# Kernel optimization log

Measured on AMD Instinct MI355X. Metric: run time of the kernel, lower is better.

Reference implementation:

```python
import jax, jax.numpy as jnp
import numpy as np

B, N, C_IN, C_OUT, R_IN, R_OUT, NUM_PSI, E = 4, 1024, 128, 256, 32, 32, 2, 65536


def psi(x, src, dst, W, b):
    # GIN-style GNN layer: aggregate neighbors via scatter-add, then linear+relu
    agg = jax.ops.segment_sum(x[src], dst, num_segments=x.shape[0])
    return jax.nn.relu((x + agg) @ W + b)


def setup_inputs() -> dict:
    key = jax.random.key(0)
    ks = jax.random.split(key, 12)
    inp = {
        'x_s': jax.random.normal(ks[0], (B * N, C_IN), jnp.float32),
        'edge_index_s': jax.random.randint(ks[1], (2, E), 0, B * N, jnp.int32),
        'x_t': jax.random.normal(ks[2], (B * N, C_IN), jnp.float32),
        'edge_index_t': jax.random.randint(ks[3], (2, E), 0, B * N, jnp.int32),
        'r': jax.random.normal(ks[4], (NUM_PSI, B, N, R_IN), jnp.float32),
        'W1': jax.random.normal(ks[5], (C_IN, C_OUT), jnp.float32) * (0.2 / np.sqrt(C_IN)),
        'b1': jnp.zeros((C_OUT,), jnp.float32),
        'Wp': jax.random.normal(ks[6], (NUM_PSI, R_IN, R_OUT), jnp.float32) * (1.0 / np.sqrt(R_IN)),
        'bp': jnp.zeros((NUM_PSI, R_OUT), jnp.float32),
        'Wm1': jax.random.normal(ks[7], (R_OUT, R_OUT), jnp.float32) * (1.0 / np.sqrt(R_OUT)),
        'bm1': jnp.zeros((R_OUT,), jnp.float32),
        'Wm2': jax.random.normal(ks[8], (R_OUT, 1), jnp.float32) * (1.0 / np.sqrt(R_OUT)),
        'bm2': jnp.zeros((1,), jnp.float32),
        'sum_weights': jnp.ones((NUM_PSI + 1,), jnp.float32),
    }
    return inp


def reference(x_s, edge_index_s, x_t, edge_index_t, r, W1, b1, Wp, bp, Wm1, bm1, Wm2, bm2, sum_weights):
    src_s, dst_s = edge_index_s[0], edge_index_s[1]
    src_t, dst_t = edge_index_t[0], edge_index_t[1]
    # psi_1 node embeddings, then dense-batch (equal-size graphs -> masks all true)
    h_s = psi(x_s, src_s, dst_s, W1, b1).reshape(B, N, C_OUT)
    h_t = psi(x_t, src_t, dst_t, W1, b1).reshape(B, N, C_OUT)
    S_hat = jnp.einsum('bsc,btc->bst', h_s, h_t)  # [B, N_s, N_t]
    S_0 = jax.nn.softmax(S_hat, axis=-1)
    S_stack = []
    for i in range(NUM_PSI):  # structurally distinct psi modules
        S = jax.nn.softmax(S_hat, axis=-1)
        r_s = r[i]  # [B, N, R_IN] random node indicators
        r_t = jnp.einsum('bst,bsr->btr', S, r_s)
        o_s = psi(r_s.reshape(B * N, R_IN), src_s, dst_s, Wp[i], bp[i]).reshape(B, N, R_OUT)
        o_t = psi(r_t.reshape(B * N, R_IN), src_t, dst_t, Wp[i], bp[i]).reshape(B, N, R_OUT)
        D = o_s[:, :, None, :] - o_t[:, None, :, :]  # [B, N_s, N_t, R_OUT]
        upd = (jax.nn.relu(D @ Wm1 + bm1) @ Wm2 + bm2)[..., 0]
        S_hat = S_hat + upd
        S_stack.append(jax.nn.softmax(S_hat, axis=-1))
    S_final = sum_weights[0] * S_0
    for i in range(NUM_PSI):
        S_final = S_final + sum_weights[i + 1] * S_stack[i]
    return jax.nn.softmax(S_final.reshape(B * N, N), axis=-1)
```

## Files before the change

### kernel.cpp

```cpp
#include <hip/hip_runtime.h>
#include <hip/hip_bf16.h>

#define NBATCH 4
#define NSEQ   1024
#define BNN    4096
#define CIN    128
#define COUT   256
#define RDIM   32
#define NEDGE  65536

__global__ void edge_hist(const int* __restrict__ ei_s, const int* __restrict__ ei_t,
                          int* __restrict__ cnt) {
    int gid = blockIdx.x * blockDim.x + threadIdx.x;
    int list = gid >> 16;
    int e = gid & (NEDGE - 1);
    const int* ei = list ? ei_t : ei_s;
    atomicAdd(&cnt[list * BNN + ei[NEDGE + e]], 1);
}

__global__ void edge_scan(const int* __restrict__ cnt, int* __restrict__ offs,
                          int* __restrict__ cursor) {
    __shared__ int sums[256];
    int list = blockIdx.x;
    int tid = threadIdx.x;
    int local[16];
    int s = 0;
#pragma unroll
    for (int k = 0; k < 16; k++) { local[k] = cnt[list * BNN + tid * 16 + k]; s += local[k]; }
    sums[tid] = s;
    __syncthreads();
    for (int off = 1; off < 256; off <<= 1) {
        int v = 0;
        if (tid >= off) v = sums[tid - off];
        __syncthreads();
        if (tid >= off) sums[tid] += v;
        __syncthreads();
    }
    int run = tid ? sums[tid - 1] : 0;
#pragma unroll
    for (int k = 0; k < 16; k++) {
        offs[list * (BNN + 1) + tid * 16 + k] = run;
        cursor[list * BNN + tid * 16 + k] = run;
        run += local[k];
    }
    if (tid == 255) offs[list * (BNN + 1) + BNN] = run;
}

__global__ void edge_place(const int* __restrict__ ei_s, const int* __restrict__ ei_t,
                           int* __restrict__ cursor, int* __restrict__ ssrc) {
    int gid = blockIdx.x * blockDim.x + threadIdx.x;
    int list = gid >> 16;
    int e = gid & (NEDGE - 1);
    const int* ei = list ? ei_t : ei_s;
    int dst = ei[NEDGE + e], src = ei[e];
    int p = atomicAdd(&cursor[list * BNN + dst], 1);
    ssrc[list * NEDGE + p] = src;
}

__global__ void gather_agg128(const float* __restrict__ x_s, const float* __restrict__ x_t,
                              const int* __restrict__ offs, const int* __restrict__ ssrc,
                              float* __restrict__ t_s, float* __restrict__ t_t) {
    __shared__ int sl[128];
    int node = blockIdx.x & (BNN - 1);
    int list = blockIdx.x >> 12;
    const float* x = list ? x_t : x_s;
    float* t = list ? t_t : t_s;
    int c = threadIdx.x;
    int beg = offs[list * (BNN + 1) + node], end = offs[list * (BNN + 1) + node + 1];
    float acc = x[(size_t)node * CIN + c];
    for (int base = beg; base < end; base += 128) {
        int cnt = min(128, end - base);
        __syncthreads();
        if (c < cnt) sl[c] = ssrc[list * NEDGE + base + c];
        __syncthreads();
        int e = 0;
        for (; e + 4 <= cnt; e += 4) {
            int n0 = sl[e], n1 = sl[e + 1], n2 = sl[e + 2], n3 = sl[e + 3];
            acc += x[(size_t)n0 * CIN + c] + x[(size_t)n1 * CIN + c]
                 + x[(size_t)n2 * CIN + c] + x[(size_t)n3 * CIN + c];
        }
        for (; e < cnt; e++) acc += x[(size_t)sl[e] * CIN + c];
    }
    t[(size_t)node * CIN + c] = acc;
}

__global__ void gather_agg32(const float* __restrict__ rs, const float* __restrict__ rtin,
                             const int* __restrict__ offs, const int* __restrict__ ssrc,
                             float* __restrict__ trs, float* __restrict__ trt) {
    int list = blockIdx.y;
    int node = blockIdx.x * 8 + (threadIdx.x >> 5);
    int c = threadIdx.x & 31;
    const float* in = list ? rtin : rs;
    float* outp = list ? trt : trs;
    int beg = offs[list * (BNN + 1) + node], end = offs[list * (BNN + 1) + node + 1];
    float acc = in[(size_t)node * RDIM + c];
    for (int e = beg; e < end; e++)
        acc += in[(size_t)ssrc[list * NEDGE + e] * RDIM + c];
    outp[(size_t)node * RDIM + c] = acc;
}

__global__ void psi1_gemm(const float* __restrict__ t_s, const float* __restrict__ t_t,
                          const float* __restrict__ W1, const float* __restrict__ b1,
                          float* __restrict__ h_s, float* __restrict__ h_t) {
    __shared__ float rows[8][CIN];
    int half = blockIdx.x >> 9;
    const float* t = half ? t_t : t_s;
    float* h = half ? h_t : h_s;
    int r0 = (blockIdx.x & 511) * 8;
    int tid = threadIdx.x;
    {
        int rr = tid >> 5, c4 = (tid & 31) << 2;
        *(float4*)&rows[rr][c4] = *(const float4*)(t + (size_t)(r0 + rr) * CIN + c4);
    }
    __syncthreads();
    float acc[8];
    float bias = b1[tid];
#pragma unroll
    for (int r = 0; r < 8; r++) acc[r] = bias;
    for (int k = 0; k < CIN; k++) {
        float w = W1[k * COUT + tid];
#pragma unroll
        for (int r = 0; r < 8; r++) acc[r] = fmaf(rows[r][k], w, acc[r]);
    }
#pragma unroll
    for (int r = 0; r < 8; r++)
        h[(size_t)(r0 + r) * COUT + tid] = fmaxf(acc[r], 0.f);
}

__global__ __launch_bounds__(256) void shat_gemm(const float* __restrict__ hs,
                                                 const float* __restrict__ ht,
                                                 float* __restrict__ Sh) {
    __shared__ float As[16][132];
    __shared__ float Bs[16][132];
    int b  = blockIdx.z;
    int s0 = blockIdx.y * 128, t0 = blockIdx.x * 128;
    const float* A  = hs + (size_t)b * NSEQ * COUT;
    const float* Bm = ht + (size_t)b * NSEQ * COUT;
    int tid = threadIdx.x;
    int tx = tid & 15, ty = tid >> 4;
    int lr = tid >> 1;
    int lk = (tid & 1) * 8;
    const float* Ap = A  + (size_t)(s0 + lr) * COUT + lk;
    const float* Bp = Bm + (size_t)(t0 + lr) * COUT + lk;
    float4 a0 = *(const float4*)(Ap);
    float4 a1 = *(const float4*)(Ap + 4);
    float4 b0 = *(const float4*)(Bp);
    float4 b1 = *(const float4*)(Bp + 4);
    float acc[8][8] = {};
    for (int kp = 0; kp < 16; kp++) {
        __syncthreads();
        As[lk + 0][lr] = a0.x; As[lk + 1][lr] = a0.y; As[lk + 2][lr] = a0.z; As[lk + 3][lr] = a0.w;
        As[lk + 4][lr] = a1.x; As[lk + 5][lr] = a1.y; As[lk + 6][lr] = a1.z; As[lk + 7][lr] = a1.w;
        Bs[lk + 0][lr] = b0.x; Bs[lk + 1][lr] = b0.y; Bs[lk + 2][lr] = b0.z; Bs[lk + 3][lr] = b0.w;
        Bs[lk + 4][lr] = b1.x; Bs[lk + 5][lr] = b1.y; Bs[lk + 6][lr] = b1.z; Bs[lk + 7][lr] = b1.w;
        __syncthreads();
        if (kp < 15) {
            a0 = *(const float4*)(Ap + (kp + 1) * 16);
            a1 = *(const float4*)(Ap + (kp + 1) * 16 + 4);
            b0 = *(const float4*)(Bp + (kp + 1) * 16);
            b1 = *(const float4*)(Bp + (kp + 1) * 16 + 4);
        }
#pragma unroll
        for (int k = 0; k < 16; k++) {
            float av[8], bv[8];
            *(float4*)&av[0] = *(const float4*)&As[k][ty * 8];
            *(float4*)&av[4] = *(const float4*)&As[k][ty * 8 + 4];
            *(float4*)&bv[0] = *(const float4*)&Bs[k][tx * 8];
            *(float4*)&bv[4] = *(const float4*)&Bs[k][tx * 8 + 4];
#pragma unroll
            for (int i = 0; i < 8; i++)
#pragma unroll
                for (int j = 0; j < 8; j++)
                    acc[i][j] = fmaf(av[i], bv[j], acc[i][j]);
        }
    }
#pragma unroll
    for (int i = 0; i < 8; i++) {
#pragma unroll
        for (int j4 = 0; j4 < 8; j4 += 4) {
            float4 v = make_float4(acc[i][j4], acc[i][j4 + 1], acc[i][j4 + 2], acc[i][j4 + 3]);
            *(float4*)(Sh + ((size_t)b * NSEQ + s0 + ty * 8 + i) * NSEQ + t0 + tx * 8 + j4) = v;
        }
    }
}

__global__ void softmax_acc2(const float* __restrict__ Sh, float* __restrict__ Sfin,
                             const float* __restrict__ sw, float* __restrict__ mstat,
                             float* __restrict__ istat, int widx, int init) {
    int row = blockIdx.x, tid = threadIdx.x;
    float4 v = *(const float4*)(Sh + (size_t)row * NSEQ + tid * 4);
    float m = fmaxf(fmaxf(v.x, v.y), fmaxf(v.z, v.w));
#pragma unroll
    for (int o = 32; o; o >>= 1) m = fmaxf(m, __shfl_xor(m, o));
    __shared__ float redm[4], reds[4];
    int wid = tid >> 6, lane = tid & 63;
    if (lane == 0) redm[wid] = m;
    __syncthreads();
    m = fmaxf(fmaxf(redm[0], redm[1]), fmaxf(redm[2], redm[3]));
    float4 e;
    e.x = __expf(v.x - m); e.y = __expf(v.y - m);
    e.z = __expf(v.z - m); e.w = __expf(v.w - m);
    float s = e.x + e.y + e.z + e.w;
#pragma unroll
    for (int o = 32; o; o >>= 1) s += __shfl_xor(s, o);
    if (lane == 0) reds[wid] = s;
    __syncthreads();
    s = reds[0] + reds[1] + reds[2] + reds[3];
    float inv = 1.0f / s;
    float w = sw[widx] * inv;
    float* fp = Sfin + (size_t)row * NSEQ + tid * 4;
    float4 f;
    if (init) {
        f = make_float4(w * e.x, w * e.y, w * e.z, w * e.w);
    } else {
        float4 old = *(const float4*)fp;
        f = make_float4(fmaf(w, e.x, old.x), fmaf(w, e.y, old.y),
                        fmaf(w, e.z, old.z), fmaf(w, e.w, old.w));
    }
    *(float4*)fp = f;
    if (tid == 0) { mstat[row] = m; istat[row] = inv; }
}

__global__ void softmax_final(const float* __restrict__ Sh, const float* __restrict__ Sfin,
                              const float* __restrict__ sw, float* __restrict__ out) {
    int row = blockIdx.x, tid = threadIdx.x;
    __shared__ float redm[4], reds[4], redm2[4], reds2[4];
    int wid = tid >> 6, lane = tid & 63;
    float4 v = *(const float4*)(Sh + (size_t)row * NSEQ + tid * 4);
    float m = fmaxf(fmaxf(v.x, v.y), fmaxf(v.z, v.w));
#pragma unroll
    for (int o = 32; o; o >>= 1) m = fmaxf(m, __shfl_xor(m, o));
    if (lane == 0) redm[wid] = m;
    __syncthreads();
    m = fmaxf(fmaxf(redm[0], redm[1]), fmaxf(redm[2], redm[3]));
    float4 e;
    e.x = __expf(v.x - m); e.y = __expf(v.y - m);
    e.z = __expf(v.z - m); e.w = __expf(v.w - m);
    float s = e.x + e.y + e.z + e.w;
#pragma unroll
    for (int o = 32; o; o >>= 1) s += __shfl_xor(s, o);
    if (lane == 0) reds[wid] = s;
    __syncthreads();
    s = reds[0] + reds[1] + reds[2] + reds[3];
    float w = sw[2] / s;
    float4 old = *(const float4*)(Sfin + (size_t)row * NSEQ + tid * 4);
    float4 f = make_float4(fmaf(w, e.x, old.x), fmaf(w, e.y, old.y),
                           fmaf(w, e.z, old.z), fmaf(w, e.w, old.w));
    float m2 = fmaxf(fmaxf(f.x, f.y), fmaxf(f.z, f.w));
#pragma unroll
    for (int o = 32; o; o >>= 1) m2 = fmaxf(m2, __shfl_xor(m2, o));
    if (lane == 0) redm2[wid] = m2;
    __syncthreads();
    m2 = fmaxf(fmaxf(redm2[0], redm2[1]), fmaxf(redm2[2], redm2[3]));
    float4 e2;
    e2.x = __expf(f.x - m2); e2.y = __expf(f.y - m2);
    e2.z = __expf(f.z - m2); e2.w = __expf(f.w - m2);
    float s2 = e2.x + e2.y + e2.z + e2.w;
#pragma unroll
    for (int o = 32; o; o >>= 1) s2 += __shfl_xor(s2, o);
    if (lane == 0) reds2[wid] = s2;
    __syncthreads();
    s2 = reds2[0] + reds2[1] + reds2[2] + reds2[3];
    float inv2 = 1.0f / s2;
    float4 sv = make_float4(e2.x * inv2, e2.y * inv2, e2.z * inv2, e2.w * inv2);
    *(float4*)(out + (size_t)row * NSEQ + tid * 4) = sv;
}

__global__ void rt_part(const float* __restrict__ Sh, const float* __restrict__ mstat,
                        const float* __restrict__ istat, const float* __restrict__ rs,
                        float* __restrict__ part) {
    __shared__ float rsld[64][33];
    __shared__ float ml[64], il[64];
    int b = blockIdx.z, t0 = blockIdx.y * 128, s0 = blockIdx.x * 64;
    int tid = threadIdx.x;
    if (tid < 64) ml[tid] = mstat[b * NSEQ + s0 + tid];
    else if (tid < 128) il[tid - 64] = istat[b * NSEQ + s0 + tid - 64];
#pragma unroll
    for (int q = 0; q < 2; q++) {
        int lid = (tid << 1) + q;
        int srow = lid >> 3, c4 = (lid & 7) << 2;
        float4 v = *(const float4*)(rs + ((size_t)b * NSEQ + s0 + srow) * RDIM + c4);
        rsld[srow][c4] = v.x; rsld[srow][c4 + 1] = v.y;
        rsld[srow][c4 + 2] = v.z; rsld[srow][c4 + 3] = v.w;
    }
    __syncthreads();
    int t = t0 + (tid & 127);
    int j0 = (tid >> 7) << 4;
    float acc[16] = {};
    const float* Sp = Sh + ((size_t)b * NSEQ + s0) * NSEQ + t;
#pragma unroll 8
    for (int s = 0; s < 64; s++) {
        float p = __expf(Sp[(size_t)s * NSEQ] - ml[s]) * il[s];
#pragma unroll
        for (int j = 0; j < 16; j++) acc[j] = fmaf(p, rsld[s][j0 + j], acc[j]);
    }
    float* pp = part + (((size_t)blockIdx.x * NBATCH + b) * NSEQ + t) * RDIM + j0;
#pragma unroll
    for (int j4 = 0; j4 < 16; j4 += 4)
        *(float4*)(pp + j4) = make_float4(acc[j4], acc[j4 + 1], acc[j4 + 2], acc[j4 + 3]);
}

__global__ void rt_reduce(const float* __restrict__ part, float* __restrict__ rt) {
    int i = blockIdx.x * blockDim.x + threadIdx.x;
    const float4* p = (const float4*)part + i;
    float4 a = make_float4(0.f, 0.f, 0.f, 0.f);
#pragma unroll
    for (int c = 0; c < 16; c++) {
        float4 v = p[(size_t)c * (BNN * RDIM / 4)];
        a.x += v.x; a.y += v.y; a.z += v.z; a.w += v.w;
    }
    ((float4*)rt)[i] = a;
}

__global__ void psi_r(const float* __restrict__ trs, const float* __restrict__ trt,
                      const float* __restrict__ Wp, const float* __restrict__ bp,
                      const float* __restrict__ Wm1, const float* __restrict__ bm1,
                      float* __restrict__ Ps, float* __restrict__ Pt) {
    __shared__ float sWp[32 * 32], sWm1[32 * 32];
    __shared__ float srow[8][33], so[8][33];
    int which = blockIdx.y;
    const float* t_r = which ? trt : trs;
    float* P = which ? Pt : Ps;
    int tid = threadIdx.x;
#pragma unroll
    for (int q = 0; q < 4; q++) {
        sWp[tid + q * 256]  = Wp[tid + q * 256];
        sWm1[tid + q * 256] = Wm1[tid + q * 256];
    }
    int g = tid >> 5, j = tid & 31;
    int row = blockIdx.x * 8 + g;
    srow[g][j] = t_r[(size_t)row * RDIM + j];
    __syncthreads();
    float acc = bp[j];
#pragma unroll
    for (int k = 0; k < 32; k++) acc = fmaf(srow[g][k], sWp[k * 32 + j], acc);
    float o = fmaxf(acc, 0.f);
    so[g][j] = o;
    __syncthreads();
    float acc2 = which ? 0.f : bm1[j];
#pragma unroll
    for (int k = 0; k < 32; k++) acc2 = fmaf(so[g][k], sWm1[k * 32 + j], acc2);
    P[(size_t)row * RDIM + j] = acc2;
}

__global__ void upd_add(const float* __restrict__ Ps, const float* __restrict__ Pt,
                        const float* __restrict__ Wm2, const float* __restrict__ bm2p,
                        float* __restrict__ Sh) {
    __shared__ float sPs[64][33], sPt[64][33];
    __shared__ float swm[32];
    int b = blockIdx.z, s0 = blockIdx.y * 64, t0 = blockIdx.x * 64;
    int tid = threadIdx.x;
#pragma unroll
    for (int q = 0; q < 2; q++) {
        int lid = (tid << 1) + q, rr = lid >> 3, c4 = (lid & 7) << 2;
        float4 a = *(const float4*)(Ps + ((size_t)b * NSEQ + s0 + rr) * RDIM + c4);
        sPs[rr][c4] = a.x; sPs[rr][c4 + 1] = a.y; sPs[rr][c4 + 2] = a.z; sPs[rr][c4 + 3] = a.w;
        float4 c = *(const float4*)(Pt + ((size_t)b * NSEQ + t0 + rr) * RDIM + c4);
        sPt[rr][c4] = c.x; sPt[rr][c4 + 1] = c.y; sPt[rr][c4 + 2] = c.z; sPt[rr][c4 + 3] = c.w;
    }
    if (tid < 32) swm[tid] = Wm2[tid];
    __syncthreads();
    float bm2 = bm2p[0];
    int tx = tid & 15, ty = tid >> 4;
    float acc[4][4] = {};
#pragma unroll
    for (int k = 0; k < 32; k++) {
        float w = swm[k];
        float ps[4], pt[4];
#pragma unroll
        for (int i = 0; i < 4; i++) ps[i] = sPs[ty * 4 + i][k];
#pragma unroll
        for (int j = 0; j < 4; j++) pt[j] = sPt[tx * 4 + j][k];
#pragma unroll
        for (int i = 0; i < 4; i++)
#pragma unroll
            for (int j = 0; j < 4; j++)
                acc[i][j] = fmaf(fmaxf(ps[i] - pt[j], 0.f), w, acc[i][j]);
    }
#pragma unroll
    for (int i = 0; i < 4; i++) {
        size_t base = ((size_t)b * NSEQ + s0 + ty * 4 + i) * NSEQ + t0 + tx * 4;
        float4 old = *(const float4*)(Sh + base);
        old.x += acc[i][0] + bm2; old.y += acc[i][1] + bm2;
        old.z += acc[i][2] + bm2; old.w += acc[i][3] + bm2;
        *(float4*)(Sh + base) = old;
    }
}

extern "C" void kernel_launch(void* const* d_in, const int* in_sizes, int n_in,
                              void* d_out, int out_size, void* d_ws, size_t ws_size,
                              hipStream_t stream) {
    const float* x_s  = (const float*)d_in[0];
    const int*   ei_s = (const int*)  d_in[1];
    const float* x_t  = (const float*)d_in[2];
    const int*   ei_t = (const int*)  d_in[3];
    const float* r    = (const float*)d_in[4];
    const float* W1   = (const float*)d_in[5];
    const float* b1   = (const float*)d_in[6];
    const float* Wp   = (const float*)d_in[7];
    const float* bp   = (const float*)d_in[8];
    const float* Wm1  = (const float*)d_in[9];
    const float* bm1  = (const float*)d_in[10];
    const float* Wm2  = (const float*)d_in[11];
    const float* bm2  = (const float*)d_in[12];
    const float* sw   = (const float*)d_in[13];
    float* out = (float*)d_out;

    float* ws = (float*)d_ws;
    float* t_s  = ws;  ws += (size_t)BNN * CIN;
    float* t_t  = ws;  ws += (size_t)BNN * CIN;
    float* h_s  = ws;  ws += (size_t)BNN * COUT;
    float* h_t  = ws;  ws += (size_t)BNN * COUT;
    float* Sh   = ws;  ws += (size_t)NBATCH * NSEQ * NSEQ;
    float* Sfin = ws;  ws += (size_t)NBATCH * NSEQ * NSEQ;
    float* mstat = ws; ws += BNN;
    float* istat = ws; ws += BNN;
    float* rt   = ws;  ws += (size_t)BNN * RDIM;
    float* trs  = ws;  ws += (size_t)BNN * RDIM;
    float* trt  = ws;  ws += (size_t)BNN * RDIM;
    float* Ps   = ws;  ws += (size_t)BNN * RDIM;
    float* Pt   = ws;  ws += (size_t)BNN * RDIM;
    int* icnt  = (int*)ws;
    int* ioffs = icnt  + 2 * BNN;
    int* icur  = ioffs + 2 * (BNN + 1);
    int* issrc = icur  + 2 * BNN;
    float* rtpart = h_s;

    hipMemsetAsync(icnt, 0, 2 * BNN * sizeof(int), stream);
    edge_hist <<<512, 256, 0, stream>>>(ei_s, ei_t, icnt);
    edge_scan <<<2, 256, 0, stream>>>(icnt, ioffs, icur);
    edge_place<<<512, 256, 0, stream>>>(ei_s, ei_t, icur, issrc);

    gather_agg128<<<8192, 128, 0, stream>>>(x_s, x_t, ioffs, issrc, t_s, t_t);
    psi1_gemm<<<1024, 256, 0, stream>>>(t_s, t_t, W1, b1, h_s, h_t);
    shat_gemm<<<dim3(8, 8, 4), 256, 0, stream>>>(h_s, h_t, Sh);

    for (int i = 0; i < 2; i++) {
        softmax_acc2<<<4096, 256, 0, stream>>>(Sh, Sfin, sw, mstat, istat, i, i == 0 ? 1 : 0);
        rt_part<<<dim3(16, 8, 4), 256, 0, stream>>>(Sh, mstat, istat,
                                                    r + (size_t)i * BNN * RDIM, rtpart);
        rt_reduce<<<128, 256, 0, stream>>>(rtpart, rt);
        gather_agg32<<<dim3(512, 2), 256, 0, stream>>>(r + (size_t)i * BNN * RDIM, rt,
                                                       ioffs, issrc, trs, trt);
        psi_r<<<dim3(512, 2), 256, 0, stream>>>(trs, trt, Wp + i * RDIM * RDIM,
                                                bp + i * RDIM, Wm1, bm1, Ps, Pt);
        upd_add<<<dim3(16, 16, 4), 256, 0, stream>>>(Ps, Pt, Wm2, bm2, Sh);
    }
    softmax_final<<<4096, 256, 0, stream>>>(Sh, Sfin, sw, out);
}
```

Before: 223.5 us.

## Keep per-stage S_hat buffers and fuse all weighted softmaxes into final pass

Instead of accumulating the weighted softmax sum into a separate Sfin buffer at every stage, each stage's S_hat is written to its own buffer and only per-row max and inverse-sum statistics are stored. A single final kernel recomputes the three softmaxes from the saved buffers, combines them and applies the outer softmax. This drops the Sfin read-modify-write passes at the cost of reading three full matrices at the end and using more workspace. The S_hat GEMM tile is also narrowed to 128x64, doubling the block count for better occupancy with less register reuse per thread.

```diff
diff --git a/kernel.cpp b/kernel.cpp
--- a/kernel.cpp
+++ b/kernel.cpp
@@ -131,62 +131,57 @@
                                                  const float* __restrict__ ht,
                                                  float* __restrict__ Sh) {
     __shared__ float As[16][132];
-    __shared__ float Bs[16][132];
+    __shared__ float Bs[16][68];
     int b  = blockIdx.z;
-    int s0 = blockIdx.y * 128, t0 = blockIdx.x * 128;
+    int s0 = blockIdx.y * 128, t0 = blockIdx.x * 64;
     const float* A  = hs + (size_t)b * NSEQ * COUT;
     const float* Bm = ht + (size_t)b * NSEQ * COUT;
     int tid = threadIdx.x;
     int tx = tid & 15, ty = tid >> 4;
-    int lr = tid >> 1;
-    int lk = (tid & 1) * 8;
-    const float* Ap = A  + (size_t)(s0 + lr) * COUT + lk;
-    const float* Bp = Bm + (size_t)(t0 + lr) * COUT + lk;
+    int lrA = tid >> 1,  lkA = (tid & 1) * 8;
+    int lrB = tid >> 2,  lkB = (tid & 3) * 4;
+    const float* Ap = A  + (size_t)(s0 + lrA) * COUT + lkA;
+    const float* Bp = Bm + (size_t)(t0 + lrB) * COUT + lkB;
     float4 a0 = *(const float4*)(Ap);
     float4 a1 = *(const float4*)(Ap + 4);
     float4 b0 = *(const float4*)(Bp);
-    float4 b1 = *(const float4*)(Bp + 4);
-    float acc[8][8] = {};
+    float acc[8][4] = {};
     for (int kp = 0; kp < 16; kp++) {
         __syncthreads();
-        As[lk + 0][lr] = a0.x; As[lk + 1][lr] = a0.y; As[lk + 2][lr] = a0.z; As[lk + 3][lr] = a0.w;
-        As[lk + 4][lr] = a1.x; As[lk + 5][lr] = a1.y; As[lk + 6][lr] = a1.z; As[lk + 7][lr] = a1.w;
-        Bs[lk + 0][lr] = b0.x; Bs[lk + 1][lr] = b0.y; Bs[lk + 2][lr] = b0.z; Bs[lk + 3][lr] = b0.w;
-        Bs[lk + 4][lr] = b1.x; Bs[lk + 5][lr] = b1.y; Bs[lk + 6][lr] = b1.z; Bs[lk + 7][lr] = b1.w;
+        As[lkA + 0][lrA] = a0.x; As[lkA + 1][lrA] = a0.y;
+        As[lkA + 2][lrA] = a0.z; As[lkA + 3][lrA] = a0.w;
+        As[lkA + 4][lrA] = a1.x; As[lkA + 5][lrA] = a1.y;
+        As[lkA + 6][lrA] = a1.z; As[lkA + 7][lrA] = a1.w;
+        Bs[lkB + 0][lrB] = b0.x; Bs[lkB + 1][lrB] = b0.y;
+        Bs[lkB + 2][lrB] = b0.z; Bs[lkB + 3][lrB] = b0.w;
         __syncthreads();
         if (kp < 15) {
             a0 = *(const float4*)(Ap + (kp + 1) * 16);
             a1 = *(const float4*)(Ap + (kp + 1) * 16 + 4);
             b0 = *(const float4*)(Bp + (kp + 1) * 16);
-            b1 = *(const float4*)(Bp + (kp + 1) * 16 + 4);
         }
 #pragma unroll
         for (int k = 0; k < 16; k++) {
-            float av[8], bv[8];
+            float av[8], bv[4];
             *(float4*)&av[0] = *(const float4*)&As[k][ty * 8];
             *(float4*)&av[4] = *(const float4*)&As[k][ty * 8 + 4];
-            *(float4*)&bv[0] = *(const float4*)&Bs[k][tx * 8];
-            *(float4*)&bv[4] = *(const float4*)&Bs[k][tx * 8 + 4];
+            *(float4*)&bv[0] = *(const float4*)&Bs[k][tx * 4];
 #pragma unroll
             for (int i = 0; i < 8; i++)
 #pragma unroll
-                for (int j = 0; j < 8; j++)
+                for (int j = 0; j < 4; j++)
                     acc[i][j] = fmaf(av[i], bv[j], acc[i][j]);
         }
     }
 #pragma unroll
     for (int i = 0; i < 8; i++) {
-#pragma unroll
-        for (int j4 = 0; j4 < 8; j4 += 4) {
-            float4 v = make_float4(acc[i][j4], acc[i][j4 + 1], acc[i][j4 + 2], acc[i][j4 + 3]);
-            *(float4*)(Sh + ((size_t)b * NSEQ + s0 + ty * 8 + i) * NSEQ + t0 + tx * 8 + j4) = v;
-        }
-    }
-}
-
-__global__ void softmax_acc2(const float* __restrict__ Sh, float* __restrict__ Sfin,
-                             const float* __restrict__ sw, float* __restrict__ mstat,
-                             float* __restrict__ istat, int widx, int init) {
+        float4 v = make_float4(acc[i][0], acc[i][1], acc[i][2], acc[i][3]);
+        *(float4*)(Sh + ((size_t)b * NSEQ + s0 + ty * 8 + i) * NSEQ + t0 + tx * 4) = v;
+    }
+}
+
+__global__ void softmax_stats(const float* __restrict__ Sh, float* __restrict__ mstat,
+                              float* __restrict__ istat) {
     int row = blockIdx.x, tid = threadIdx.x;
     float4 v = *(const float4*)(Sh + (size_t)row * NSEQ + tid * 4);
     float m = fmaxf(fmaxf(v.x, v.y), fmaxf(v.z, v.w));
@@ -197,72 +192,71 @@
     if (lane == 0) redm[wid] = m;
     __syncthreads();
     m = fmaxf(fmaxf(redm[0], redm[1]), fmaxf(redm[2], redm[3]));
-    float4 e;
-    e.x = __expf(v.x - m); e.y = __expf(v.y - m);
-    e.z = __expf(v.z - m); e.w = __expf(v.w - m);
-    float s = e.x + e.y + e.z + e.w;
+    float s = __expf(v.x - m) + __expf(v.y - m) + __expf(v.z - m) + __expf(v.w - m);
 #pragma unroll
     for (int o = 32; o; o >>= 1) s += __shfl_xor(s, o);
     if (lane == 0) reds[wid] = s;
     __syncthreads();
-    s = reds[0] + reds[1] + reds[2] + reds[3];
-    float inv = 1.0f / s;
-    float w = sw[widx] * inv;
-    float* fp = Sfin + (size_t)row * NSEQ + tid * 4;
+    if (tid == 0) {
+        float tot = reds[0] + reds[1] + reds[2] + reds[3];
+        mstat[row] = m;
+        istat[row] = 1.0f / tot;
+    }
+}
+
+__global__ void softmax_final3(const float* __restrict__ Sh0, const float* __restrict__ Sh1,
+                               const float* __restrict__ Sh2, const float* __restrict__ m0a,
+                               const float* __restrict__ i0a, const float* __restrict__ m1a,
+                               const float* __restrict__ i1a, const float* __restrict__ sw,
+                               float* __restrict__ out) {
+    int row = blockIdx.x, tid = threadIdx.x;
+    __shared__ float red[4];
+    int wid = tid >> 6, lane = tid & 63;
+    float4 v0 = *(const float4*)(Sh0 + (size_t)row * NSEQ + tid * 4);
+    float4 v1 = *(const float4*)(Sh1 + (size_t)row * NSEQ + tid * 4);
+    float4 v2 = *(const float4*)(Sh2 + (size_t)row * NSEQ + tid * 4);
+    float m2 = fmaxf(fmaxf(v2.x, v2.y), fmaxf(v2.z, v2.w));
+#pragma unroll
+    for (int o = 32; o; o >>= 1) m2 = fmaxf(m2, __shfl_xor(m2, o));
+    if (lane == 0) red[wid] = m2;
+    __syncthreads();
+    m2 = fmaxf(fmaxf(red[0], red[1]), fmaxf(red[2], red[3]));
+    __syncthreads();
+    float4 e2;
+    e2.x = __expf(v2.x - m2); e2.y = __expf(v2.y - m2);
+    e2.z = __expf(v2.z - m2); e2.w = __expf(v2.w - m2);
+    float s2 = e2.x + e2.y + e2.z + e2.w;
+#pragma unroll
+    for (int o = 32; o; o >>= 1) s2 += __shfl_xor(s2, o);
+    if (lane == 0) red[wid] = s2;
+    __syncthreads();
+    s2 = red[0] + red[1] + red[2] + red[3];
+    __syncthreads();
+    float w0 = sw[0] * i0a[row], w1 = sw[1] * i1a[row], w2 = sw[2] / s2;
+    float m0 = m0a[row], m1 = m1a[row];
     float4 f;
-    if (init) {
-        f = make_float4(w * e.x, w * e.y, w * e.z, w * e.w);
-    } else {
-        float4 old = *(const float4*)fp;
-        f = make_float4(fmaf(w, e.x, old.x), fmaf(w, e.y, old.y),
-                        fmaf(w, e.z, old.z), fmaf(w, e.w, old.w));
-    }
-    *(float4*)fp = f;
-    if (tid == 0) { mstat[row] = m; istat[row] = inv; }
-}
-
-__global__ void softmax_final(const float* __restrict__ Sh, const float* __restrict__ Sfin,
-                              const float* __restrict__ sw, float* __restrict__ out) {
-    int row = blockIdx.x, tid = threadIdx.x;
-    __shared__ float redm[4], reds[4], redm2[4], reds2[4];
-    int wid = tid >> 6, lane = tid & 63;
-    float4 v = *(const float4*)(Sh + (size_t)row * NSEQ + tid * 4);
-    float m = fmaxf(fmaxf(v.x, v.y), fmaxf(v.z, v.w));
-#pragma unroll
-    for (int o = 32; o; o >>= 1) m = fmaxf(m, __shfl_xor(m, o));
-    if (lane == 0) redm[wid] = m;
-    __syncthreads();
-    m = fmaxf(fmaxf(redm[0], redm[1]), fmaxf(redm[2], redm[3]));
-    float4 e;
-    e.x = __expf(v.x - m); e.y = __expf(v.y - m);
-    e.z = __expf(v.z - m); e.w = __expf(v.w - m);
-    float s = e.x + e.y + e.z + e.w;
-#pragma unroll
-    for (int o = 32; o; o >>= 1) s += __shfl_xor(s, o);
-    if (lane == 0) reds[wid] = s;
-    __syncthreads();
-    s = reds[0] + reds[1] + reds[2] + reds[3];
-    float w = sw[2] / s;
-    float4 old = *(const float4*)(Sfin + (size_t)row * NSEQ + tid * 4);
-    float4 f = make_float4(fmaf(w, e.x, old.x), fmaf(w, e.y, old.y),
-                           fmaf(w, e.z, old.z), fmaf(w, e.w, old.w));
-    float m2 = fmaxf(fmaxf(f.x, f.y), fmaxf(f.z, f.w));
-#pragma unroll
-    for (int o = 32; o; o >>= 1) m2 = fmaxf(m2, __shfl_xor(m2, o));
-    if (lane == 0) redm2[wid] = m2;
-    __syncthreads();
-    m2 = fmaxf(fmaxf(redm2[0], redm2[1]), fmaxf(redm2[2], redm2[3]));
-    float4 e2;
-    e2.x = __expf(f.x - m2); e2.y = __expf(f.y - m2);
-    e2.z = __expf(f.z - m2); e2.w = __expf(f.w - m2);
-    float s2 = e2.x + e2.y + e2.z + e2.w;
-#pragma unroll
-    for (int o = 32; o; o >>= 1) s2 += __shfl_xor(s2, o);
-    if (lane == 0) reds2[wid] = s2;
-    __syncthreads();
-    s2 = reds2[0] + reds2[1] + reds2[2] + reds2[3];
-    float inv2 = 1.0f / s2;
-    float4 sv = make_float4(e2.x * inv2, e2.y * inv2, e2.z * inv2, e2.w * inv2);
+    f.x = fmaf(w0, __expf(v0.x - m0), fmaf(w1, __expf(v1.x - m1), w2 * e2.x));
+    f.y = fmaf(w0, __expf(v0.y - m0), fmaf(w1, __expf(v1.y - m1), w2 * e2.y));
+    f.z = fmaf(w0, __expf(v0.z - m0), fmaf(w1, __expf(v1.z - m1), w2 * e2.z));
+    f.w = fmaf(w0, __expf(v0.w - m0), fmaf(w1, __expf(v1.w - m1), w2 * e2.w));
+    float mf = fmaxf(fmaxf(f.x, f.y), fmaxf(f.z, f.w));
+#pragma unroll
+    for (int o = 32; o; o >>= 1) mf = fmaxf(mf, __shfl_xor(mf, o));
+    if (lane == 0) red[wid] = mf;
+    __syncthreads();
+    mf = fmaxf(fmaxf(red[0], red[1]), fmaxf(red[2], red[3]));
+    __syncthreads();
+    float4 ef;
+    ef.x = __expf(f.x - mf); ef.y = __expf(f.y - mf);
+    ef.z = __expf(f.z - mf); ef.w = __expf(f.w - mf);
+    float sf = ef.x + ef.y + ef.z + ef.w;
+#pragma unroll
+    for (int o = 32; o; o >>= 1) sf += __shfl_xor(sf, o);
+    if (lane == 0) red[wid] = sf;
+    __syncthreads();
+    sf = red[0] + red[1] + red[2] + red[3];
+    float inv = 1.0f / sf;
+    float4 sv = make_float4(ef.x * inv, ef.y * inv, ef.z * inv, ef.w * inv);
     *(float4*)(out + (size_t)row * NSEQ + tid * 4) = sv;
 }
 
@@ -345,7 +339,7 @@
 
 __global__ void upd_add(const float* __restrict__ Ps, const float* __restrict__ Pt,
                         const float* __restrict__ Wm2, const float* __restrict__ bm2p,
-                        float* __restrict__ Sh) {
+                        const float* __restrict__ Shin, float* __restrict__ Shout) {
     __shared__ float sPs[64][33], sPt[64][33];
     __shared__ float swm[32];
     int b = blockIdx.z, s0 = blockIdx.y * 64, t0 = blockIdx.x * 64;
@@ -380,10 +374,10 @@
 #pragma unroll
     for (int i = 0; i < 4; i++) {
         size_t base = ((size_t)b * NSEQ + s0 + ty * 4 + i) * NSEQ + t0 + tx * 4;
-        float4 old = *(const float4*)(Sh + base);
+        float4 old = *(const float4*)(Shin + base);
         old.x += acc[i][0] + bm2; old.y += acc[i][1] + bm2;
         old.z += acc[i][2] + bm2; old.w += acc[i][3] + bm2;
-        *(float4*)(Sh + base) = old;
+        *(float4*)(Shout + base) = old;
     }
 }
 
@@ -411,10 +405,11 @@
     float* t_t  = ws;  ws += (size_t)BNN * CIN;
     float* h_s  = ws;  ws += (size_t)BNN * COUT;
     float* h_t  = ws;  ws += (size_t)BNN * COUT;
-    float* Sh   = ws;  ws += (size_t)NBATCH * NSEQ * NSEQ;
-    float* Sfin = ws;  ws += (size_t)NBATCH * NSEQ * NSEQ;
-    float* mstat = ws; ws += BNN;
-    float* istat = ws; ws += BNN;
+    float* Sh0  = ws;  ws += (size_t)NBATCH * NSEQ * NSEQ;
+    float* Sh1  = ws;  ws += (size_t)NBATCH * NSEQ * NSEQ;
+    float* Sh2  = ws;  ws += (size_t)NBATCH * NSEQ * NSEQ;
+    float* mstat = ws; ws += 2 * BNN;
+    float* istat = ws; ws += 2 * BNN;
     float* rt   = ws;  ws += (size_t)BNN * RDIM;
     float* trs  = ws;  ws += (size_t)BNN * RDIM;
     float* trt  = ws;  ws += (size_t)BNN * RDIM;
@@ -426,6 +421,8 @@
     int* issrc = icur  + 2 * BNN;
     float* rtpart = h_s;
 
+    float* ShA[3] = {Sh0, Sh1, Sh2};
+
     hipMemsetAsync(icnt, 0, 2 * BNN * sizeof(int), stream);
     edge_hist <<<512, 256, 0, stream>>>(ei_s, ei_t, icnt);
     edge_scan <<<2, 256, 0, stream>>>(icnt, ioffs, icur);
@@ -433,18 +430,19 @@
 
     gather_agg128<<<8192, 128, 0, stream>>>(x_s, x_t, ioffs, issrc, t_s, t_t);
     psi1_gemm<<<1024, 256, 0, stream>>>(t_s, t_t, W1, b1, h_s, h_t);
-    shat_gemm<<<dim3(8, 8, 4), 256, 0, stream>>>(h_s, h_t, Sh);
+    shat_gemm<<<dim3(16, 8, 4), 256, 0, stream>>>(h_s, h_t, Sh0);
 
     for (int i = 0; i < 2; i++) {
-        softmax_acc2<<<4096, 256, 0, stream>>>(Sh, Sfin, sw, mstat, istat, i, i == 0 ? 1 : 0);
-        rt_part<<<dim3(16, 8, 4), 256, 0, stream>>>(Sh, mstat, istat,
+        softmax_stats<<<4096, 256, 0, stream>>>(ShA[i], mstat + i * BNN, istat + i * BNN);
+        rt_part<<<dim3(16, 8, 4), 256, 0, stream>>>(ShA[i], mstat + i * BNN, istat + i * BNN,
                                                     r + (size_t)i * BNN * RDIM, rtpart);
         rt_reduce<<<128, 256, 0, stream>>>(rtpart, rt);
         gather_agg32<<<dim3(512, 2), 256, 0, stream>>>(r + (size_t)i * BNN * RDIM, rt,
                                                        ioffs, issrc, trs, trt);
         psi_r<<<dim3(512, 2), 256, 0, stream>>>(trs, trt, Wp + i * RDIM * RDIM,
                                                 bp + i * RDIM, Wm1, bm1, Ps, Pt);
-        upd_add<<<dim3(16, 16, 4), 256, 0, stream>>>(Ps, Pt, Wm2, bm2, Sh);
-    }
-    softmax_final<<<4096, 256, 0, stream>>>(Sh, Sfin, sw, out);
-}
+        upd_add<<<dim3(16, 16, 4), 256, 0, stream>>>(Ps, Pt, Wm2, bm2, ShA[i], ShA[i + 1]);
+    }
+    softmax_final3<<<4096, 256, 0, stream>>>(Sh0, Sh1, Sh2, mstat, istat,
+                                             mstat + BNN, istat + BNN, sw, out);
+}
```

Result: faster. 214.5 us (-4.0%).
